# Kernel tuning notes

Hardware: AMD Instinct MI355X
Metric: run time of the kernel (lower is better)

The kernel has to match this reference:

```python
import jax, jax.numpy as jnp
import numpy as np

B, N, C = 2, 6, 80
FH, FW = 16, 44
D = 112
NX = NY = 128
NZ = 1
OGH, OGW = 256, 704
D_BOUND = (2.0, 58.0, 0.5)
VOXEL_SIZE = np.array([0.8, 0.8, 8.0], dtype=np.float32)
VOXEL_COORD = np.array([-51.2 + 0.4, -51.2 + 0.4, -5.0 + 4.0], dtype=np.float32)
VOXEL_NUM = np.array([NX, NY, NZ], dtype=np.int32)


def setup_inputs() -> dict:
    key = jax.random.key(0)
    k1, k2 = jax.random.split(key)
    context = jax.random.normal(k1, (B * N, C, FH, FW), jnp.float32)
    depth_logits = jax.random.normal(k2, (B * N, D, FH, FW), jnp.float32)
    # realistic camera matrices (random matrices would not be invertible / physical)
    intrin = np.tile(np.eye(4, dtype=np.float32), (B, N, 1, 1))
    intrin[..., 0, 0] = 560.0
    intrin[..., 1, 1] = 560.0
    intrin[..., 0, 2] = OGW / 2.0
    intrin[..., 1, 2] = OGH / 2.0
    ida = np.tile(np.eye(4, dtype=np.float32), (B, N, 1, 1))
    s2e = np.tile(np.eye(4, dtype=np.float32), (B, N, 1, 1))
    # cam axes (x right, y down, z forward) -> ego axes (x fwd, y left, z up)
    M = np.array([[0., 0., 1.], [-1., 0., 0.], [0., -1., 0.]], dtype=np.float32)
    for n in range(N):
        yaw = 2.0 * np.pi * n / N
        cy, sy = np.cos(yaw), np.sin(yaw)
        R = np.array([[cy, -sy, 0.], [sy, cy, 0.], [0., 0., 1.]], dtype=np.float32)
        s2e[:, n, :3, :3] = R @ M
        s2e[:, n, :3, 3] = np.array([1.5 * cy, 1.5 * sy, 1.6], dtype=np.float32)
    bda = np.tile(np.eye(4, dtype=np.float32), (B, 1, 1))
    return dict(context=context, depth_logits=depth_logits,
                sensor2ego_mat=jnp.asarray(s2e), intrin_mat=jnp.asarray(intrin),
                ida_mat=jnp.asarray(ida), bda_mat=jnp.asarray(bda))


def _frustum():
    # [D, FH, FW, 4] pixel-plane frustum: (u, v, depth, 1)
    d = jnp.arange(D_BOUND[0], D_BOUND[1], D_BOUND[2], dtype=jnp.float32) + D_BOUND[2] / 2.0
    d = jnp.broadcast_to(d[:, None, None], (D, FH, FW))
    xs = jnp.broadcast_to(jnp.linspace(0.0, OGW - 1.0, FW)[None, None, :], (D, FH, FW))
    ys = jnp.broadcast_to(jnp.linspace(0.0, OGH - 1.0, FH)[None, :, None], (D, FH, FW))
    return jnp.stack([xs, ys, d, jnp.ones_like(d)], -1)


def reference(context, depth_logits, sensor2ego_mat, intrin_mat, ida_mat, bda_mat):
    # ---- get_geometry ----
    pts = _frustum()[None, None, ..., None]                       # [1,1,D,FH,FW,4,1]
    ida_inv = jnp.linalg.inv(ida_mat).reshape(B, N, 1, 1, 1, 4, 4)
    pts = ida_inv @ pts
    pts = jnp.concatenate([pts[..., :2, :] * pts[..., 2:3, :], pts[..., 2:, :]], axis=-2)
    combine = (sensor2ego_mat @ jnp.linalg.inv(intrin_mat)).reshape(B, N, 1, 1, 1, 4, 4)
    pts = combine @ pts
    bda = bda_mat.reshape(B, 1, 1, 1, 1, 4, 4)
    geom = (bda @ pts)[..., :3, 0]                                # [B,N,D,FH,FW,3] ego coords

    # ---- voxel indices ----
    vsize = jnp.asarray(VOXEL_SIZE)
    vcoord = jnp.asarray(VOXEL_COORD)
    vnum = jnp.asarray(VOXEL_NUM)
    idx = jnp.floor((geom - (vcoord - vsize / 2.0)) / vsize).astype(jnp.int32)
    valid = jnp.all((idx >= 0) & (idx < vnum), axis=-1)           # [B,N,D,FH,FW]

    # ---- lift: depth-weighted outer product ----
    depth = jax.nn.softmax(depth_logits, axis=1).reshape(B, N, D, FH, FW)
    ctx = context.reshape(B, N, C, FH, FW)
    feat = jnp.einsum('bndhw,bnchw->bndhwc', depth, ctx)          # [B,N,D,FH,FW,C]
    feat = feat * valid[..., None]

    # ---- splat: scatter-add into BEV grid ----
    b_idx = jnp.arange(B, dtype=jnp.int32)[:, None, None, None, None]
    lin = b_idx * (NY * NX) + idx[..., 1] * NX + idx[..., 0]
    lin = jnp.where(valid, lin, 0)                                # invalid feats already zeroed
    bev = jax.ops.segment_sum(feat.reshape(-1, C), lin.reshape(-1),
                              num_segments=B * NY * NX)
    return bev.reshape(B, NY, NX, C).transpose(0, 3, 1, 2)        # [B,C,NY,NX]
```

## Files before the change

kernel.cpp:

```cpp
#include <hip/hip_runtime.h>
#include <hip/hip_bf16.h>
#include <math.h>

#define B_ 2
#define N_ 6
#define C_ 80
#define FH_ 16
#define FW_ 44
#define D_ 112
#define NX_ 128
#define NY_ 128
#define HW_ (FH_ * FW_)
#define NCOL (B_ * N_ * HW_)
#define NCELL (B_ * NY_ * NX_)
#define MAXT (NCOL * D_)
#define GB_CELLS 16
#define NCB 2112
#define NTB 2640

typedef __hip_bfloat16 bf16;
typedef unsigned short u16;

__device__ __forceinline__ float loadf(const void* p, int i, int isbf) {
  if (isbf) return __bfloat162float(((const bf16*)p)[i]);
  return ((const float*)p)[i];
}

__device__ void inv4(const float m[16], float invOut[16]) {
  float inv[16];
  inv[0]  =  m[5]*m[10]*m[15] - m[5]*m[11]*m[14] - m[9]*m[6]*m[15] + m[9]*m[7]*m[14] + m[13]*m[6]*m[11] - m[13]*m[7]*m[10];
  inv[4]  = -m[4]*m[10]*m[15] + m[4]*m[11]*m[14] + m[8]*m[6]*m[15] - m[8]*m[7]*m[14] - m[12]*m[6]*m[11] + m[12]*m[7]*m[10];
  inv[8]  =  m[4]*m[9]*m[15]  - m[4]*m[11]*m[13] - m[8]*m[5]*m[15] + m[8]*m[7]*m[13] + m[12]*m[5]*m[11] - m[12]*m[7]*m[9];
  inv[12] = -m[4]*m[9]*m[14]  + m[4]*m[10]*m[13] + m[8]*m[5]*m[14] - m[8]*m[6]*m[13] - m[12]*m[5]*m[10] + m[12]*m[6]*m[9];
  inv[1]  = -m[1]*m[10]*m[15] + m[1]*m[11]*m[14] + m[9]*m[2]*m[15] - m[9]*m[3]*m[14] - m[13]*m[2]*m[11] + m[13]*m[3]*m[10];
  inv[5]  =  m[0]*m[10]*m[15] - m[0]*m[11]*m[14] - m[8]*m[2]*m[15] + m[8]*m[3]*m[14] + m[12]*m[2]*m[11] - m[12]*m[3]*m[10];
  inv[9]  = -m[0]*m[9]*m[15]  + m[0]*m[11]*m[13] + m[8]*m[1]*m[15] - m[8]*m[3]*m[13] - m[12]*m[1]*m[11] + m[12]*m[3]*m[9];
  inv[13] =  m[0]*m[9]*m[14]  - m[0]*m[10]*m[13] - m[8]*m[1]*m[14] + m[8]*m[2]*m[13] + m[12]*m[1]*m[10] - m[12]*m[2]*m[9];
  inv[2]  =  m[1]*m[6]*m[15]  - m[1]*m[7]*m[14]  - m[5]*m[2]*m[15] + m[5]*m[3]*m[14] + m[13]*m[2]*m[7]  - m[13]*m[3]*m[6];
  inv[6]  = -m[0]*m[6]*m[15]  + m[0]*m[7]*m[14]  + m[4]*m[2]*m[15] - m[4]*m[3]*m[14] - m[12]*m[2]*m[7]  + m[12]*m[3]*m[6];
  inv[10] =  m[0]*m[5]*m[15]  - m[0]*m[7]*m[13]  - m[4]*m[1]*m[15] + m[4]*m[3]*m[13] + m[12]*m[1]*m[7]  - m[12]*m[3]*m[5];
  inv[14] = -m[0]*m[5]*m[14]  + m[0]*m[6]*m[13]  + m[4]*m[1]*m[14] - m[4]*m[2]*m[13] - m[12]*m[1]*m[6]  + m[12]*m[2]*m[5];
  inv[3]  = -m[1]*m[6]*m[11]  + m[1]*m[7]*m[10]  + m[5]*m[2]*m[11] - m[5]*m[3]*m[10] - m[9]*m[2]*m[7]   + m[9]*m[3]*m[6];
  inv[7]  =  m[0]*m[6]*m[11]  - m[0]*m[7]*m[10]  - m[4]*m[2]*m[11] + m[4]*m[3]*m[10] + m[8]*m[2]*m[7]   - m[8]*m[3]*m[6];
  inv[11] = -m[0]*m[5]*m[11]  + m[0]*m[7]*m[9]   + m[4]*m[1]*m[11] - m[4]*m[3]*m[9]  - m[8]*m[1]*m[7]   + m[8]*m[3]*m[5];
  inv[15] =  m[0]*m[5]*m[10]  - m[0]*m[6]*m[9]   - m[4]*m[1]*m[10] + m[4]*m[2]*m[9]  + m[8]*m[1]*m[6]   - m[8]*m[2]*m[5];
  float det = m[0]*inv[0] + m[1]*inv[4] + m[2]*inv[8] + m[3]*inv[12];
  det = 1.0f / det;
  for (int i = 0; i < 16; i++) invOut[i] = inv[i] * det;
}

__device__ void mul4(const float A[16], const float Bm[16], float Cm[16]) {
  for (int i = 0; i < 4; i++)
    for (int j = 0; j < 4; j++) {
      float s = 0.f;
      for (int k = 0; k < 4; k++) s += A[i * 4 + k] * Bm[k * 4 + j];
      Cm[i * 4 + j] = s;
    }
}

__device__ __forceinline__ int geom_cell(const float* __restrict__ mats,
                                         int bn, int h, int w, int d) {
  const float* Ai = mats + bn * 32;
  const float* M = mats + bn * 32 + 16;
  float u = (float)w * (703.0f / 43.0f);
  float v = (float)h * 17.0f;
  float dep = 2.25f + 0.5f * (float)d;
  float p0 = ((Ai[0] * u + Ai[1] * v) + Ai[2] * dep) + Ai[3];
  float p1 = ((Ai[4] * u + Ai[5] * v) + Ai[6] * dep) + Ai[7];
  float p2 = ((Ai[8] * u + Ai[9] * v) + Ai[10] * dep) + Ai[11];
  float p3 = ((Ai[12] * u + Ai[13] * v) + Ai[14] * dep) + Ai[15];
  float q0 = p0 * p2, q1 = p1 * p2;
  float gx = ((M[0] * q0 + M[1] * q1) + M[2] * p2) + M[3] * p3;
  float gy = ((M[4] * q0 + M[5] * q1) + M[6] * p2) + M[7] * p3;
  float gz = ((M[8] * q0 + M[9] * q1) + M[10] * p2) + M[11] * p3;
  int ix = (int)floorf((gx + 51.2f) / 0.8f);
  int iy = (int)floorf((gy + 51.2f) / 0.8f);
  int iz = (int)floorf((gz + 5.0f) / 8.0f);
  bool valid = (ix >= 0) && (ix < NX_) && (iy >= 0) && (iy < NY_) && (iz == 0);
  int b = bn / N_;
  return valid ? (b * (NY_ * NX_) + iy * NX_ + ix) : -1;
}

__global__ __launch_bounds__(256) void lss_prep(
    const void* __restrict__ logits,
    const void* __restrict__ s2e, const void* __restrict__ intrin,
    const void* __restrict__ ida, const void* __restrict__ bda,
    float* __restrict__ mats, int* __restrict__ flags,
    int* __restrict__ counts) {
  const int t = threadIdx.x;
  const int blk = blockIdx.x;
  for (int i = blk * 256 + t; i < NCELL; i += 33 * 256) counts[i] = 0;
  if (blk != 0) return;

  __shared__ int s_cnt;
  __shared__ int s_mats_bf;
  if (t == 0) s_cnt = 0;
  __syncthreads();
  {
    const unsigned short* u = (const unsigned short*)logits;
    unsigned short v = u[2 * t];
    int e = (v >> 7) & 0xFF;
    if (v == 0 || (e >= 110 && e <= 136)) atomicAdd(&s_cnt, 1);
  }
  __syncthreads();
  if (t == 0) {
    flags[0] = (s_cnt > 170) ? 1 : 0;
    float v = ((const float*)intrin)[0];
    s_mats_bf = (v > 100.f && v < 1.0e6f) ? 0 : 1;
    flags[1] = s_mats_bf;
  }
  __syncthreads();
  const int mbf = s_mats_bf;
  if (t < B_ * N_) {
    int b = t / N_;
    float S[16], I[16], A[16], Bd[16], Iinv[16], Ainv[16], Cm[16], M[16];
    for (int i = 0; i < 16; i++) {
      S[i]  = loadf(s2e,    t * 16 + i, mbf);
      I[i]  = loadf(intrin, t * 16 + i, mbf);
      A[i]  = loadf(ida,    t * 16 + i, mbf);
      Bd[i] = loadf(bda,    b * 16 + i, mbf);
    }
    inv4(I, Iinv);
    inv4(A, Ainv);
    mul4(S, Iinv, Cm);
    mul4(Bd, Cm, M);
    for (int i = 0; i < 16; i++) { mats[t * 32 + i] = Ainv[i]; mats[t * 32 + 16 + i] = M[i]; }
  }
}

__global__ __launch_bounds__(256) void lss_count(
    const void* __restrict__ ctx, const float* __restrict__ mats,
    const int* __restrict__ flags, int* __restrict__ counts,
    float* __restrict__ ctx_t) {
  const int t = threadIdx.x;
  const int blk = blockIdx.x;

  if (blk >= NCB) {
    const int tbf = flags[0];
    const int i = (blk - NCB) * 256 + t;
    int col = i / C_, c = i - col * C_;
    int bn = col / HW_, r = col - bn * HW_;
    int h = r / FW_, w = r - h * FW_;
    ctx_t[i] = loadf(ctx, ((bn * C_ + c) * FH_ + h) * FW_ + w, tbf);
    return;
  }

  const int col = blk * 4 + (t >> 6);
  const int ln = t & 63;
  const int w = col % FW_;
  const int h = (col / FW_) % FH_;
  const int bn = col / (FW_ * FH_);
  int c0 = geom_cell(mats, bn, h, w, ln);
  int c1 = (ln < D_ - 64) ? geom_cell(mats, bn, h, w, ln + 64) : -3;
  int p0 = __shfl_up(c0, 1);
  int p1 = __shfl_up(c1, 1);
  int c63 = __shfl(c0, 63);
  if (ln == 0) p1 = c63;
  if (c0 >= 0 && (ln == 0 || p0 != c0)) atomicAdd(&counts[c0], 1);
  if (c1 >= 0 && p1 != c1) atomicAdd(&counts[c1], 1);
}

__global__ __launch_bounds__(1024) void lss_scan(const int* __restrict__ counts,
                                                 int* __restrict__ offsets,
                                                 int* __restrict__ cursors) {
  __shared__ int s[1024];
  const int t = threadIdx.x;
  const int base = t * 32;
  int local[32];
  int sum = 0;
  for (int j = 0; j < 32; j++) { local[j] = counts[base + j]; sum += local[j]; }
  s[t] = sum;
  __syncthreads();
  for (int st = 1; st < 1024; st <<= 1) {
    int v = (t >= st) ? s[t - st] : 0;
    __syncthreads();
    s[t] += v;
    __syncthreads();
  }
  int run = s[t] - sum;
  for (int j = 0; j < 32; j++) {
    offsets[base + j] = run;
    cursors[base + j] = run;
    run += local[j];
  }
}

__global__ __launch_bounds__(64) void lss_fill(
    const void* __restrict__ logits, const float* __restrict__ mats,
    const int* __restrict__ flags, int* __restrict__ cursors,
    u16* __restrict__ colids, float* __restrict__ wts) {
  const int tid = threadIdx.x;
  const int col = blockIdx.x;
  const int w = col % FW_;
  const int h = (col / FW_) % FH_;
  const int bn = col / (FW_ * FH_);
  const int tbf = flags[0];

  __shared__ float s_w[D_];
  __shared__ int s_cell[D_];

  const int base = ((bn * D_) * FH_ + h) * FW_ + w;
  float l0 = loadf(logits, base + tid * (FH_ * FW_), tbf);
  float l1 = (tid < D_ - 64) ? loadf(logits, base + (tid + 64) * (FH_ * FW_), tbf) : -1e30f;
  float m = fmaxf(l0, l1);
  for (int s = 32; s > 0; s >>= 1) m = fmaxf(m, __shfl_xor(m, s));
  float e0 = expf(l0 - m);
  float e1 = (tid < D_ - 64) ? expf(l1 - m) : 0.f;
  float sum = e0 + e1;
  for (int s = 32; s > 0; s >>= 1) sum += __shfl_xor(sum, s);
  float inv_sum = 1.0f / sum;

  s_w[tid] = e0;
  s_cell[tid] = geom_cell(mats, bn, h, w, tid);
  if (tid < D_ - 64) {
    s_w[tid + 64] = e1;
    s_cell[tid + 64] = geom_cell(mats, bn, h, w, tid + 64);
  }
  __syncthreads();

  for (int d = tid; d < D_; d += 64) {
    int vcell = s_cell[d];
    if (vcell >= 0 && (d == 0 || s_cell[d - 1] != vcell)) {
      float acc = s_w[d];
      for (int j = d + 1; j < D_ && s_cell[j] == vcell; ++j) acc += s_w[j];
      int pos = atomicAdd(&cursors[vcell], 1);
      colids[pos] = (u16)col;
      wts[pos] = acc * inv_sum;
    }
  }
}

__global__ __launch_bounds__(1024) void lss_gather(
    const float* __restrict__ ctx_t, const int* __restrict__ counts,
    const int* __restrict__ offsets, const u16* __restrict__ colids,
    const float* __restrict__ wts, const int* __restrict__ flags,
    void* __restrict__ out) {
  __shared__ float s_out[GB_CELLS * 84];
  const int tid = threadIdx.x;
  const int wv = tid >> 6;
  const int ln = tid & 63;
  const int sl = ln >> 2;
  const int g = ln & 3;
  const int cell = blockIdx.x * GB_CELLS + wv;
  const int n = counts[cell];
  const int off = offsets[cell];

  float acc[20];
#pragma unroll
  for (int i = 0; i < 20; i++) acc[i] = 0.f;

  for (int j = sl; j < n; j += 16) {
    int colj = colids[off + j];
    float wj = wts[off + j];
    const float4* cp = (const float4*)(ctx_t + colj * C_ + g * 20);
#pragma unroll
    for (int q = 0; q < 5; q++) {
      float4 v = cp[q];
      acc[q * 4 + 0] += wj * v.x;
      acc[q * 4 + 1] += wj * v.y;
      acc[q * 4 + 2] += wj * v.z;
      acc[q * 4 + 3] += wj * v.w;
    }
  }
#pragma unroll
  for (int msk = 4; msk <= 32; msk <<= 1) {
#pragma unroll
    for (int i = 0; i < 20; i++) acc[i] += __shfl_xor(acc[i], msk);
  }
  if (sl == 0) {
#pragma unroll
    for (int i = 0; i < 20; i++) s_out[wv * 84 + g * 20 + i] = acc[i];
  }
  __syncthreads();

  const int x = tid & 15;
  const int c0 = tid >> 4;
  const int cell0 = blockIdx.x * GB_CELLS;
  const int b = cell0 >> 14;
  const int yx0 = cell0 & 16383;
  if (flags[0]) {
    bf16* o = (bf16*)out;
    o[(size_t)(b * C_ + c0) * (NY_ * NX_) + yx0 + x] = __float2bfloat16(s_out[x * 84 + c0]);
    if (c0 < 16)
      o[(size_t)(b * C_ + 64 + c0) * (NY_ * NX_) + yx0 + x] = __float2bfloat16(s_out[x * 84 + 64 + c0]);
  } else {
    float* o = (float*)out;
    o[(size_t)(b * C_ + c0) * (NY_ * NX_) + yx0 + x] = s_out[x * 84 + c0];
    if (c0 < 16)
      o[(size_t)(b * C_ + 64 + c0) * (NY_ * NX_) + yx0 + x] = s_out[x * 84 + 64 + c0];
  }
}

extern "C" void kernel_launch(void* const* d_in, const int* in_sizes, int n_in,
                              void* d_out, int out_size, void* d_ws, size_t ws_size,
                              hipStream_t stream) {
  const void* ctx = d_in[0];
  const void* logits = d_in[1];
  const void* s2e = d_in[2];
  const void* intrin = d_in[3];
  const void* ida = d_in[4];
  const void* bda = d_in[5];

  float* wsf = (float*)d_ws;
  int* flags   = (int*)wsf;
  float* mats  = wsf + 16;
  int* counts  = (int*)(wsf + 512);
  int* offsets = counts + NCELL;
  int* cursors = offsets + NCELL;
  float* ctx_t = (float*)(cursors + NCELL);
  float* wts   = ctx_t + NCOL * C_;
  u16* colids  = (u16*)(wts + MAXT);

  lss_prep<<<33, 256, 0, stream>>>(logits, s2e, intrin, ida, bda, mats, flags, counts);
  lss_count<<<NCB + NTB, 256, 0, stream>>>(ctx, mats, flags, counts, ctx_t);
  lss_scan<<<1, 1024, 0, stream>>>(counts, offsets, cursors);
  lss_fill<<<NCOL, 64, 0, stream>>>(logits, mats, flags, cursors, colids, wts);
  lss_gather<<<NCELL / GB_CELLS, 1024, 0, stream>>>(ctx_t, counts, offsets, colids, wts, flags, d_out);
}
```

Before: 178.2 us.

## Fuse prep and scan into count kernel with last-block scan; pack fill blocks

Drops the separate prep and single-block scan kernels. Every count block now builds the camera matrices in shared memory, and the last block to finish (found through an atomic done counter) runs the exclusive prefix scan over the cell counts. The counts are cleared with a memset, and the fill kernel now handles four columns per 256-thread block instead of one column per 64-thread block. The aim is to cut launch overhead and small serial kernels. In exchange, every block recomputes the matrix inverses, and the tail scan runs on only 256 threads.

```diff
diff --git a/kernel.cpp b/kernel.cpp
--- a/kernel.cpp
+++ b/kernel.cpp
@@ -81,36 +81,9 @@
   return valid ? (b * (NY_ * NX_) + iy * NX_ + ix) : -1;
 }
 
-__global__ __launch_bounds__(256) void lss_prep(
-    const void* __restrict__ logits,
-    const void* __restrict__ s2e, const void* __restrict__ intrin,
-    const void* __restrict__ ida, const void* __restrict__ bda,
-    float* __restrict__ mats, int* __restrict__ flags,
-    int* __restrict__ counts) {
-  const int t = threadIdx.x;
-  const int blk = blockIdx.x;
-  for (int i = blk * 256 + t; i < NCELL; i += 33 * 256) counts[i] = 0;
-  if (blk != 0) return;
-
-  __shared__ int s_cnt;
-  __shared__ int s_mats_bf;
-  if (t == 0) s_cnt = 0;
-  __syncthreads();
-  {
-    const unsigned short* u = (const unsigned short*)logits;
-    unsigned short v = u[2 * t];
-    int e = (v >> 7) & 0xFF;
-    if (v == 0 || (e >= 110 && e <= 136)) atomicAdd(&s_cnt, 1);
-  }
-  __syncthreads();
-  if (t == 0) {
-    flags[0] = (s_cnt > 170) ? 1 : 0;
-    float v = ((const float*)intrin)[0];
-    s_mats_bf = (v > 100.f && v < 1.0e6f) ? 0 : 1;
-    flags[1] = s_mats_bf;
-  }
-  __syncthreads();
-  const int mbf = s_mats_bf;
+__device__ __forceinline__ void build_mats(
+    const void* s2e, const void* intrin, const void* ida, const void* bda,
+    int mbf, int t, float* dst) {
   if (t < B_ * N_) {
     int b = t / N_;
     float S[16], I[16], A[16], Bd[16], Iinv[16], Ainv[16], Cm[16], M[16];
@@ -124,80 +97,142 @@
     inv4(A, Ainv);
     mul4(S, Iinv, Cm);
     mul4(Bd, Cm, M);
-    for (int i = 0; i < 16; i++) { mats[t * 32 + i] = Ainv[i]; mats[t * 32 + 16 + i] = M[i]; }
+    for (int i = 0; i < 16; i++) { dst[t * 32 + i] = Ainv[i]; dst[t * 32 + 16 + i] = M[i]; }
   }
 }
 
 __global__ __launch_bounds__(256) void lss_count(
-    const void* __restrict__ ctx, const float* __restrict__ mats,
-    const int* __restrict__ flags, int* __restrict__ counts,
+    const void* __restrict__ ctx, const void* __restrict__ logits,
+    const void* __restrict__ s2e, const void* __restrict__ intrin,
+    const void* __restrict__ ida, const void* __restrict__ bda,
+    float* __restrict__ mats_g, int* __restrict__ flags_g,
+    int* __restrict__ counts, int* __restrict__ offsets,
+    int* __restrict__ cursors, int* __restrict__ done,
     float* __restrict__ ctx_t) {
   const int t = threadIdx.x;
   const int blk = blockIdx.x;
+  const int ln = t & 63;
+  const int wv = t >> 6;
+
+  __shared__ int s_b[4];
 
   if (blk >= NCB) {
-    const int tbf = flags[0];
+    const unsigned short* u = (const unsigned short*)logits;
+    unsigned short v = u[2 * t];
+    int e = (v >> 7) & 0xFF;
+    unsigned long long bm = __ballot(v == 0 || (e >= 110 && e <= 136));
+    if (ln == 0) s_b[wv] = __popcll(bm);
+    __syncthreads();
+    const int tbf = (s_b[0] + s_b[1] + s_b[2] + s_b[3] > 170) ? 1 : 0;
     const int i = (blk - NCB) * 256 + t;
     int col = i / C_, c = i - col * C_;
     int bn = col / HW_, r = col - bn * HW_;
-    int h = r / FW_, w = r - h * FW_;
-    ctx_t[i] = loadf(ctx, ((bn * C_ + c) * FH_ + h) * FW_ + w, tbf);
+    int h = r / FW_, w2 = r - h * FW_;
+    ctx_t[i] = loadf(ctx, ((bn * C_ + c) * FH_ + h) * FW_ + w2, tbf);
     return;
   }
 
-  const int col = blk * 4 + (t >> 6);
-  const int ln = t & 63;
-  const int w = col % FW_;
-  const int h = (col / FW_) % FH_;
-  const int bn = col / (FW_ * FH_);
-  int c0 = geom_cell(mats, bn, h, w, ln);
-  int c1 = (ln < D_ - 64) ? geom_cell(mats, bn, h, w, ln + 64) : -3;
-  int p0 = __shfl_up(c0, 1);
-  int p1 = __shfl_up(c1, 1);
-  int c63 = __shfl(c0, 63);
-  if (ln == 0) p1 = c63;
-  if (c0 >= 0 && (ln == 0 || p0 != c0)) atomicAdd(&counts[c0], 1);
-  if (c1 >= 0 && p1 != c1) atomicAdd(&counts[c1], 1);
-}
-
-__global__ __launch_bounds__(1024) void lss_scan(const int* __restrict__ counts,
-                                                 int* __restrict__ offsets,
-                                                 int* __restrict__ cursors) {
-  __shared__ int s[1024];
-  const int t = threadIdx.x;
-  const int base = t * 32;
-  int local[32];
-  int sum = 0;
-  for (int j = 0; j < 32; j++) { local[j] = counts[base + j]; sum += local[j]; }
-  s[t] = sum;
-  __syncthreads();
-  for (int st = 1; st < 1024; st <<= 1) {
-    int v = (t >= st) ? s[t - st] : 0;
-    __syncthreads();
-    s[t] += v;
-    __syncthreads();
-  }
-  int run = s[t] - sum;
-  for (int j = 0; j < 32; j++) {
-    offsets[base + j] = run;
-    cursors[base + j] = run;
-    run += local[j];
-  }
-}
-
-__global__ __launch_bounds__(64) void lss_fill(
+  __shared__ float s_mats[B_ * N_ * 32];
+  const float iv0 = ((const float*)intrin)[0];
+  const int mbf = (iv0 > 100.f && iv0 < 1.0e6f) ? 0 : 1;
+  build_mats(s2e, intrin, ida, bda, mbf, t, s_mats);
+
+  int pred = 0;
+  if (blk == 0) {
+    const unsigned short* u = (const unsigned short*)logits;
+    unsigned short v = u[2 * t];
+    int e = (v >> 7) & 0xFF;
+    pred = (v == 0 || (e >= 110 && e <= 136)) ? 1 : 0;
+  }
+  unsigned long long bm = __ballot(pred);
+  if (ln == 0) s_b[wv] = __popcll(bm);
+  __syncthreads();
+  if (blk == 0) {
+    if (t == 0) {
+      flags_g[0] = (s_b[0] + s_b[1] + s_b[2] + s_b[3] > 170) ? 1 : 0;
+      flags_g[1] = mbf;
+    }
+    if (t < B_ * N_)
+      for (int i = 0; i < 32; i++) mats_g[t * 32 + i] = s_mats[t * 32 + i];
+  }
+
+  {
+    const int col = blk * 4 + wv;
+    const int w = col % FW_;
+    const int h = (col / FW_) % FH_;
+    const int bn = col / (FW_ * FH_);
+    int c0 = geom_cell(s_mats, bn, h, w, ln);
+    int c1 = (ln < D_ - 64) ? geom_cell(s_mats, bn, h, w, ln + 64) : -3;
+    int p0 = __shfl_up(c0, 1);
+    int p1 = __shfl_up(c1, 1);
+    int c63 = __shfl(c0, 63);
+    if (ln == 0) p1 = c63;
+    if (c0 >= 0 && (ln == 0 || p0 != c0)) atomicAdd(&counts[c0], 1);
+    if (c1 >= 0 && p1 != c1) atomicAdd(&counts[c1], 1);
+  }
+
+  __syncthreads();
+  __shared__ int s_last;
+  if (t == 0) {
+    __threadfence();
+    s_last = (atomicAdd(done, 1) == NCB - 1);
+  }
+  __syncthreads();
+  if (!s_last) return;
+  __threadfence();
+
+  const int cb = t * 128;
+#define LDC(k) __hip_atomic_load(&counts[cb + j + (k)], __ATOMIC_RELAXED, __HIP_MEMORY_SCOPE_AGENT)
+  int tot = 0;
+#pragma unroll 2
+  for (int j = 0; j < 128; j += 8) {
+    int a0 = LDC(0), a1 = LDC(1), a2 = LDC(2), a3 = LDC(3);
+    int a4 = LDC(4), a5 = LDC(5), a6 = LDC(6), a7 = LDC(7);
+    tot += ((a0 + a1) + (a2 + a3)) + ((a4 + a5) + (a6 + a7));
+  }
+  int incl = tot;
+#pragma unroll
+  for (int s = 1; s < 64; s <<= 1) {
+    int u2 = __shfl_up(incl, s);
+    if (ln >= s) incl += u2;
+  }
+  __shared__ int s_wsum[4];
+  if (ln == 63) s_wsum[wv] = incl;
+  __syncthreads();
+  int wbase = 0;
+  for (int k = 0; k < wv; k++) wbase += s_wsum[k];
+  int run = wbase + incl - tot;
+#pragma unroll 2
+  for (int j = 0; j < 128; j += 8) {
+    int a0 = LDC(0), a1 = LDC(1), a2 = LDC(2), a3 = LDC(3);
+    int a4 = LDC(4), a5 = LDC(5), a6 = LDC(6), a7 = LDC(7);
+    offsets[cb + j + 0] = run; cursors[cb + j + 0] = run; run += a0;
+    offsets[cb + j + 1] = run; cursors[cb + j + 1] = run; run += a1;
+    offsets[cb + j + 2] = run; cursors[cb + j + 2] = run; run += a2;
+    offsets[cb + j + 3] = run; cursors[cb + j + 3] = run; run += a3;
+    offsets[cb + j + 4] = run; cursors[cb + j + 4] = run; run += a4;
+    offsets[cb + j + 5] = run; cursors[cb + j + 5] = run; run += a5;
+    offsets[cb + j + 6] = run; cursors[cb + j + 6] = run; run += a6;
+    offsets[cb + j + 7] = run; cursors[cb + j + 7] = run; run += a7;
+  }
+#undef LDC
+}
+
+__global__ __launch_bounds__(256) void lss_fill(
     const void* __restrict__ logits, const float* __restrict__ mats,
     const int* __restrict__ flags, int* __restrict__ cursors,
     u16* __restrict__ colids, float* __restrict__ wts) {
-  const int tid = threadIdx.x;
-  const int col = blockIdx.x;
+  const int t = threadIdx.x;
+  const int wv = t >> 6;
+  const int tid = t & 63;
+  const int col = blockIdx.x * 4 + wv;
   const int w = col % FW_;
   const int h = (col / FW_) % FH_;
   const int bn = col / (FW_ * FH_);
   const int tbf = flags[0];
 
-  __shared__ float s_w[D_];
-  __shared__ int s_cell[D_];
+  __shared__ float s_w[4][D_];
+  __shared__ int s_cell[4][D_];
 
   const int base = ((bn * D_) * FH_ + h) * FW_ + w;
   float l0 = loadf(logits, base + tid * (FH_ * FW_), tbf);
@@ -210,19 +245,19 @@
   for (int s = 32; s > 0; s >>= 1) sum += __shfl_xor(sum, s);
   float inv_sum = 1.0f / sum;
 
-  s_w[tid] = e0;
-  s_cell[tid] = geom_cell(mats, bn, h, w, tid);
+  s_w[wv][tid] = e0;
+  s_cell[wv][tid] = geom_cell(mats, bn, h, w, tid);
   if (tid < D_ - 64) {
-    s_w[tid + 64] = e1;
-    s_cell[tid + 64] = geom_cell(mats, bn, h, w, tid + 64);
+    s_w[wv][tid + 64] = e1;
+    s_cell[wv][tid + 64] = geom_cell(mats, bn, h, w, tid + 64);
   }
   __syncthreads();
 
   for (int d = tid; d < D_; d += 64) {
-    int vcell = s_cell[d];
-    if (vcell >= 0 && (d == 0 || s_cell[d - 1] != vcell)) {
-      float acc = s_w[d];
-      for (int j = d + 1; j < D_ && s_cell[j] == vcell; ++j) acc += s_w[j];
+    int vcell = s_cell[wv][d];
+    if (vcell >= 0 && (d == 0 || s_cell[wv][d - 1] != vcell)) {
+      float acc = s_w[wv][d];
+      for (int j = d + 1; j < D_ && s_cell[wv][j] == vcell; ++j) acc += s_w[wv][j];
       int pos = atomicAdd(&cursors[vcell], 1);
       colids[pos] = (u16)col;
       wts[pos] = acc * inv_sum;
@@ -305,15 +340,18 @@
   int* flags   = (int*)wsf;
   float* mats  = wsf + 16;
   int* counts  = (int*)(wsf + 512);
-  int* offsets = counts + NCELL;
+  int* done    = counts + NCELL;
+  int* offsets = counts + NCELL + 16;
   int* cursors = offsets + NCELL;
   float* ctx_t = (float*)(cursors + NCELL);
   float* wts   = ctx_t + NCOL * C_;
   u16* colids  = (u16*)(wts + MAXT);
-
-  lss_prep<<<33, 256, 0, stream>>>(logits, s2e, intrin, ida, bda, mats, flags, counts);
-  lss_count<<<NCB + NTB, 256, 0, stream>>>(ctx, mats, flags, counts, ctx_t);
-  lss_scan<<<1, 1024, 0, stream>>>(counts, offsets, cursors);
-  lss_fill<<<NCOL, 64, 0, stream>>>(logits, mats, flags, cursors, colids, wts);
+  (void)done;
+
+  hipMemsetAsync(counts, 0, (NCELL + 16) * sizeof(int), stream);
+  lss_count<<<NCB + NTB, 256, 0, stream>>>(ctx, logits, s2e, intrin, ida, bda,
+                                           mats, flags, counts, offsets,
+                                           cursors, counts + NCELL, ctx_t);
+  lss_fill<<<NCOL / 4, 256, 0, stream>>>(logits, mats, flags, cursors, colids, wts);
   lss_gather<<<NCELL / GB_CELLS, 1024, 0, stream>>>(ctx_t, counts, offsets, colids, wts, flags, d_out);
 }
```

After: 232.8 us. 1.31x slower.
